# Optimization experiments

Hardware: AMD Instinct MI355X
Metric: run time of the kernel (lower is better)

Reference implementation:

```python
import jax, jax.numpy as jnp
import numpy as np

B, N, ENC = 64, 49, 2048
DEC, ATT, EMB, V, TP1 = 512, 512, 300, 10000, 31


def setup_inputs() -> dict:
    key = jax.random.key(0)
    ks = jax.random.split(key, 20)
    s = 0.02
    inp = {
        "features": jax.random.normal(ks[0], (B, N, ENC), jnp.float32),
        "captions": jax.random.randint(ks[1], (B, TP1), 0, V, jnp.int64),
        "emb": jax.random.normal(ks[2], (V, EMB), jnp.float32) * s,
        "U_w": jax.random.normal(ks[3], (ATT, ENC), jnp.float32) * s,
        "U_b": jnp.zeros((ATT,), jnp.float32),
        "W_w": jax.random.normal(ks[4], (ATT, DEC), jnp.float32) * s,
        "W_b": jnp.zeros((ATT,), jnp.float32),
        "A_w": jax.random.normal(ks[5], (1, ATT), jnp.float32) * s,
        "A_b": jnp.zeros((1,), jnp.float32),
        "initH_w": jax.random.normal(ks[6], (DEC, ENC), jnp.float32) * s,
        "initH_b": jnp.zeros((DEC,), jnp.float32),
        "initC_w": jax.random.normal(ks[7], (DEC, ENC), jnp.float32) * s,
        "initC_b": jnp.zeros((DEC,), jnp.float32),
        "ih_w": jax.random.normal(ks[8], (4 * DEC, EMB + ENC), jnp.float32) * s,
        "ih_b": jnp.zeros((4 * DEC,), jnp.float32),
        "hh_w": jax.random.normal(ks[9], (4 * DEC, DEC), jnp.float32) * s,
        "hh_b": jnp.zeros((4 * DEC,), jnp.float32),
        "fcn_w": jax.random.normal(ks[10], (V, DEC), jnp.float32) * s,
        "fcn_b": jnp.zeros((V,), jnp.float32),
    }
    return inp


def reference(features, captions, emb, U_w, U_b, W_w, W_b, A_w, A_b,
              initH_w, initH_b, initC_w, initC_b,
              ih_w, ih_b, hh_w, hh_b, fcn_w, fcn_b):
    # embeds: [B, T+1, EMB]  (prembed lookup, frozen table)
    embeds = emb[captions]
    T = captions.shape[1] - 1  # static

    # init_hidden_state
    mean_f = features.mean(axis=1)                  # [B, ENC]
    h0 = mean_f @ initH_w.T + initH_b               # [B, DEC]
    c0 = mean_f @ initC_w.T + initC_b

    # U(features) is step-invariant: hoist out of the loop (same math)
    u_hs = jnp.einsum('bne,ae->bna', features, U_w) + U_b  # [B, N, ATT]

    xs = jnp.swapaxes(embeds[:, :T], 0, 1)          # [T, B, EMB]

    def step(carry, x):
        h, c = carry
        # additive attention
        w_ah = h @ W_w.T + W_b                       # [B, ATT]
        comb = jnp.tanh(u_hs + w_ah[:, None, :])     # [B, N, ATT]
        scores = jnp.einsum('bna,a->bn', comb, A_w[0]) + A_b[0]
        alpha = jax.nn.softmax(scores, axis=1)       # [B, N]
        context = jnp.einsum('bn,bne->be', alpha, features)  # [B, ENC]
        # LSTMCell
        lstm_in = jnp.concatenate([x, context], axis=1)
        gates = lstm_in @ ih_w.T + ih_b + h @ hh_w.T + hh_b
        i, f, g, o = jnp.split(gates, 4, axis=1)
        i, f, o = jax.nn.sigmoid(i), jax.nn.sigmoid(f), jax.nn.sigmoid(o)
        g = jnp.tanh(g)
        c = f * c + i * g
        h = o * jnp.tanh(c)
        # dropout in eval mode = identity
        out = h @ fcn_w.T + fcn_b                    # [B, V]
        return (h, c), (out, alpha)

    _, (preds, alphas) = jax.lax.scan(step, (h0, c0), xs)
    preds = jnp.swapaxes(preds, 0, 1)                # [B, T, V]
    alphas = jnp.swapaxes(alphas, 0, 1)              # [B, T, N]
    return preds, alphas
```

## Files before the change

### kernel.cpp

```cpp
#include <hip/hip_runtime.h>
#include <math.h>

#define B 64
#define NN 49
#define ENC 2048
#define DEC 512
#define ATT 512
#define EMB 300
#define VOC 10000
#define TT 30

typedef __attribute__((ext_vector_type(4))) float f32x4;
typedef __attribute__((ext_vector_type(4))) short s16x4;
typedef __attribute__((ext_vector_type(8))) short s16x8;
typedef unsigned short u16;

__device__ __forceinline__ float fast_tanh(float x) {
    float e = __expf(2.f * x);
    return 1.f - 2.f / (e + 1.f);
}
__device__ __forceinline__ float sigmoidf(float x) {
    return 1.f / (1.f + __expf(-x));
}
__device__ __forceinline__ u16 f2bf(float x) {
    unsigned u = __float_as_uint(x);
    unsigned r = u + 0x7FFFu + ((u >> 16) & 1u);
    return (u16)(r >> 16);
}
__device__ __forceinline__ float bf2f(u16 u) {
    return __uint_as_float((unsigned)u << 16);
}
__device__ __forceinline__ void split_bf16(float x, short& hi, short& lo) {
    u16 h = f2bf(x);
    float hf = __uint_as_float((unsigned)h << 16);
    hi = (short)h;
    lo = (short)f2bf(x - hf);
}
__device__ __forceinline__ s16x8 ld8(const short* p) {
    s16x4 a = *(const s16x4*)p;
    s16x4 b = *(const s16x4*)(p + 4);
    return __builtin_shufflevector(a, b, 0, 1, 2, 3, 4, 5, 6, 7);
}
__device__ __forceinline__ int xcd_swz(int bid, int nwg) {
    const int q = nwg >> 3, r = nwg & 7;
    const int xcd = bid & 7, idx = bid >> 3;
    return ((xcd < r) ? xcd * (q + 1) : r * (q + 1) + (xcd - r) * q) + idx;
}

__global__ __launch_bounds__(512) void mfma_cat3(
    const u16* __restrict__ fhi,
    const float* __restrict__ U_w, const float* __restrict__ U_b,
    const u16* __restrict__ ihw_h, const u16* __restrict__ ihw_l,
    u16* __restrict__ uhs16, u16* __restrict__ fW16, int M)
{
    __shared__ short Ah[128][40];
    __shared__ short Bh[128][40];
    __shared__ short Bl[128][40];

    const int tid = threadIdx.x;
    const int nwg = gridDim.x * gridDim.y;
    const int swz = xcd_swz(blockIdx.y * gridDim.x + blockIdx.x, nwg);
    const int m0 = (swz / gridDim.x) * 128;
    const int n0 = (swz % gridDim.x) * 128;
    const int wid = tid >> 6, lane = tid & 63;
    const int wm = wid >> 2, wn = wid & 3;
    const int lrow = lane & 15;
    const int lko = (lane >> 4) * 8;
    const int srow = tid >> 2;
    const int sk = (tid & 3) * 8;

    const int gc = n0 + srow;
    const int gr = m0 + srow;
    const u16* ahp = fhi + (size_t)gr * 2048;

    f32x4 acc[4][2];
    #pragma unroll
    for (int i = 0; i < 4; ++i)
        #pragma unroll
        for (int j = 0; j < 2; ++j)
            acc[i][j] = (f32x4){0.f, 0.f, 0.f, 0.f};

    for (int kt = 0; kt < 64; ++kt) {
        const int kb0 = kt * 32 + sk;
        {
            s16x8 vh = {0,0,0,0,0,0,0,0};
            if (gr < M) vh = *(const s16x8*)(ahp + kb0);
            *(s16x8*)&Ah[srow][sk] = vh;
        }
        if (n0 < 512) {
            const float* bp = U_w + (size_t)gc * 2048;
            float4 x0 = *(const float4*)(bp + kb0);
            float4 x1 = *(const float4*)(bp + kb0 + 4);
            float v[8] = {x0.x, x0.y, x0.z, x0.w, x1.x, x1.y, x1.z, x1.w};
            s16x4 h0, h1, l0, l1;
            #pragma unroll
            for (int j = 0; j < 4; ++j) { short h, l; split_bf16(v[j], h, l); h0[j] = h; l0[j] = l; }
            #pragma unroll
            for (int j = 0; j < 4; ++j) { short h, l; split_bf16(v[4 + j], h, l); h1[j] = h; l1[j] = l; }
            *(s16x4*)&Bh[srow][sk] = h0; *(s16x4*)&Bh[srow][sk + 4] = h1;
            *(s16x4*)&Bl[srow][sk] = l0; *(s16x4*)&Bl[srow][sk + 4] = l1;
        } else {
            *(s16x8*)&Bh[srow][sk] = *(const s16x8*)(ihw_h + (size_t)(gc - 512) * 2048 + kb0);
            *(s16x8*)&Bl[srow][sk] = *(const s16x8*)(ihw_l + (size_t)(gc - 512) * 2048 + kb0);
        }
        __syncthreads();

        s16x8 bh[2], bl[2];
        #pragma unroll
        for (int nr = 0; nr < 2; ++nr) {
            const int col = wn * 32 + nr * 16 + lrow;
            bh[nr] = ld8(&Bh[col][lko]);
            bl[nr] = ld8(&Bl[col][lko]);
        }
        #pragma unroll
        for (int mr = 0; mr < 4; ++mr) {
            const int row = wm * 64 + mr * 16 + lrow;
            s16x8 ah = ld8(&Ah[row][lko]);
            #pragma unroll
            for (int nr = 0; nr < 2; ++nr) {
                acc[mr][nr] = __builtin_amdgcn_mfma_f32_16x16x32_bf16(ah, bh[nr], acc[mr][nr], 0, 0, 0);
                acc[mr][nr] = __builtin_amdgcn_mfma_f32_16x16x32_bf16(ah, bl[nr], acc[mr][nr], 0, 0, 0);
            }
        }
        __syncthreads();
    }

    #pragma unroll
    for (int mr = 0; mr < 4; ++mr) {
        #pragma unroll
        for (int nr = 0; nr < 2; ++nr) {
            #pragma unroll
            for (int r = 0; r < 4; ++r) {
                const int row = m0 + wm * 64 + mr * 16 + (lane >> 4) * 4 + r;
                const int col = n0 + wn * 32 + nr * 16 + (lane & 15);
                if (row < M) {
                    if (col < 512)
                        uhs16[(size_t)row * 512 + col] = f2bf(acc[mr][nr][r] + U_b[col]);
                    else
                        fW16[(size_t)row * 2048 + (col - 512)] = f2bf(acc[mr][nr][r]);
                }
            }
        }
    }
}

__global__ __launch_bounds__(512) void mfma_prex(
    const int* __restrict__ cap,
    const float* __restrict__ emb,
    const float* __restrict__ ih_w,
    const float* __restrict__ bias2,
    float* __restrict__ pre_x)
{
    __shared__ short Ah[128][40];
    __shared__ short Al[128][40];
    __shared__ short Bh[128][40];
    __shared__ short Bl[128][40];

    const int tid = threadIdx.x;
    const int m0 = blockIdx.y * 128, n0 = blockIdx.x * 128;
    const int wid = tid >> 6, lane = tid & 63;
    const int wm = wid >> 2, wn = wid & 3;
    const int lrow = lane & 15;
    const int lko = (lane >> 4) * 8;
    const int srow = tid >> 2;
    const int sk = (tid & 3) * 8;

    const int gr = m0 + srow;
    const int tt = gr >> 6, bbs = gr & 63;
    const float* ap = emb + (size_t)cap[bbs * 31 + tt] * 300;
    const int gc = n0 + srow;
    const float* bp = ih_w + (size_t)gc * 2348;

    f32x4 acc[4][2];
    #pragma unroll
    for (int i = 0; i < 4; ++i)
        #pragma unroll
        for (int j = 0; j < 2; ++j)
            acc[i][j] = (f32x4){0.f, 0.f, 0.f, 0.f};

    for (int kt = 0; kt < 10; ++kt) {
        const int kb0 = kt * 32 + sk;
        {
            float v[8];
            if (kb0 + 7 < 300) {
                float4 x0 = *(const float4*)(ap + kb0);
                float4 x1 = *(const float4*)(ap + kb0 + 4);
                v[0] = x0.x; v[1] = x0.y; v[2] = x0.z; v[3] = x0.w;
                v[4] = x1.x; v[5] = x1.y; v[6] = x1.z; v[7] = x1.w;
            } else {
                #pragma unroll
                for (int j = 0; j < 8; ++j)
                    v[j] = (kb0 + j < 300) ? ap[kb0 + j] : 0.f;
            }
            s16x4 h0, h1, l0, l1;
            #pragma unroll
            for (int j = 0; j < 4; ++j) { short h, l; split_bf16(v[j], h, l); h0[j] = h; l0[j] = l; }
            #pragma unroll
            for (int j = 0; j < 4; ++j) { short h, l; split_bf16(v[4 + j], h, l); h1[j] = h; l1[j] = l; }
            *(s16x4*)&Ah[srow][sk] = h0; *(s16x4*)&Ah[srow][sk + 4] = h1;
            *(s16x4*)&Al[srow][sk] = l0; *(s16x4*)&Al[srow][sk + 4] = l1;
        }
        {
            float v[8];
            if (kb0 + 7 < 300) {
                float4 x0 = *(const float4*)(bp + kb0);
                float4 x1 = *(const float4*)(bp + kb0 + 4);
                v[0] = x0.x; v[1] = x0.y; v[2] = x0.z; v[3] = x0.w;
                v[4] = x1.x; v[5] = x1.y; v[6] = x1.z; v[7] = x1.w;
            } else {
                #pragma unroll
                for (int j = 0; j < 8; ++j)
                    v[j] = (kb0 + j < 300) ? bp[kb0 + j] : 0.f;
            }
            s16x4 h0, h1, l0, l1;
            #pragma unroll
            for (int j = 0; j < 4; ++j) { short h, l; split_bf16(v[j], h, l); h0[j] = h; l0[j] = l; }
            #pragma unroll
            for (int j = 0; j < 4; ++j) { short h, l; split_bf16(v[4 + j], h, l); h1[j] = h; l1[j] = l; }
            *(s16x4*)&Bh[srow][sk] = h0; *(s16x4*)&Bh[srow][sk + 4] = h1;
            *(s16x4*)&Bl[srow][sk] = l0; *(s16x4*)&Bl[srow][sk + 4] = l1;
        }
        __syncthreads();

        s16x8 bh[2], bl[2];
        #pragma unroll
        for (int nr = 0; nr < 2; ++nr) {
            const int col = wn * 32 + nr * 16 + lrow;
            bh[nr] = ld8(&Bh[col][lko]);
            bl[nr] = ld8(&Bl[col][lko]);
        }
        #pragma unroll
        for (int mr = 0; mr < 4; ++mr) {
            const int row = wm * 64 + mr * 16 + lrow;
            s16x8 ah = ld8(&Ah[row][lko]);
            s16x8 al = ld8(&Al[row][lko]);
            #pragma unroll
            for (int nr = 0; nr < 2; ++nr) {
                acc[mr][nr] = __builtin_amdgcn_mfma_f32_16x16x32_bf16(ah, bh[nr], acc[mr][nr], 0, 0, 0);
                acc[mr][nr] = __builtin_amdgcn_mfma_f32_16x16x32_bf16(ah, bl[nr], acc[mr][nr], 0, 0, 0);
                acc[mr][nr] = __builtin_amdgcn_mfma_f32_16x16x32_bf16(al, bh[nr], acc[mr][nr], 0, 0, 0);
            }
        }
        __syncthreads();
    }

    #pragma unroll
    for (int mr = 0; mr < 4; ++mr) {
        #pragma unroll
        for (int nr = 0; nr < 2; ++nr) {
            #pragma unroll
            for (int r = 0; r < 4; ++r) {
                const int row = m0 + wm * 64 + mr * 16 + (lane >> 4) * 4 + r;
                const int col = n0 + wn * 32 + nr * 16 + (lane & 15);
                pre_x[(size_t)row * 2048 + col] = acc[mr][nr][r] + bias2[col];
            }
        }
    }
}

__global__ __launch_bounds__(512) void mfma_pre3(
    const u16* __restrict__ Ahg,
    const u16* __restrict__ Bhg,
    const float* __restrict__ bias,
    float* __restrict__ C, int M, int N)
{
    __shared__ short Ah[128][40];
    __shared__ short Bh[128][40];

    const int tid = threadIdx.x;
    const int nwg = gridDim.x * gridDim.y;
    const int swz = xcd_swz(blockIdx.y * gridDim.x + blockIdx.x, nwg);
    const int m0 = (swz / gridDim.x) * 128;
    const int n0 = (swz % gridDim.x) * 128;
    const int wid = tid >> 6, lane = tid & 63;
    const int wm = wid >> 2, wn = wid & 3;
    const int lrow = lane & 15;
    const int lko = (lane >> 4) * 8;
    const int srow = tid >> 2;
    const int sk = (tid & 3) * 8;

    f32x4 acc[4][2];
    #pragma unroll
    for (int i = 0; i < 4; ++i)
        #pragma unroll
        for (int j = 0; j < 2; ++j)
            acc[i][j] = (f32x4){0.f, 0.f, 0.f, 0.f};

    for (int kt = 0; kt < 16; ++kt) {
        const int kb0 = kt * 32 + sk;
        {
            const int gr = m0 + srow;
            s16x8 vh = {0,0,0,0,0,0,0,0};
            if (gr < M) vh = *(const s16x8*)(Ahg + (size_t)gr * 512 + kb0);
            *(s16x8*)&Ah[srow][sk] = vh;
        }
        {
            const int gc = n0 + srow;
            s16x8 vh = {0,0,0,0,0,0,0,0};
            if (gc < N) vh = *(const s16x8*)(Bhg + (size_t)gc * 512 + kb0);
            *(s16x8*)&Bh[srow][sk] = vh;
        }
        __syncthreads();

        s16x8 bh[2];
        #pragma unroll
        for (int nr = 0; nr < 2; ++nr) {
            const int col = wn * 32 + nr * 16 + lrow;
            bh[nr] = ld8(&Bh[col][lko]);
        }
        #pragma unroll
        for (int mr = 0; mr < 4; ++mr) {
            const int row = wm * 64 + mr * 16 + lrow;
            s16x8 ah = ld8(&Ah[row][lko]);
            #pragma unroll
            for (int nr = 0; nr < 2; ++nr)
                acc[mr][nr] = __builtin_amdgcn_mfma_f32_16x16x32_bf16(ah, bh[nr], acc[mr][nr], 0, 0, 0);
        }
        __syncthreads();
    }

    #pragma unroll
    for (int mr = 0; mr < 4; ++mr) {
        #pragma unroll
        for (int nr = 0; nr < 2; ++nr) {
            #pragma unroll
            for (int r = 0; r < 4; ++r) {
                const int row = m0 + wm * 64 + mr * 16 + (lane >> 4) * 4 + r;
                const int col = n0 + wn * 32 + nr * 16 + (lane & 15);
                if (row < M && col < N) {
                    const float val = acc[mr][nr][r] + bias[col];
                    const int t = row >> 6, bb = row & 63;
                    C[(size_t)bb * (TT * VOC) + (size_t)t * VOC + col] = val;
                }
            }
        }
    }
}

__global__ __launch_bounds__(256) void k_mean(const float* __restrict__ f,
                                              float* __restrict__ mean_f)
{
    const int b = blockIdx.x;
    for (int e = threadIdx.x; e < ENC; e += 256) {
        float s = 0.f;
        for (int n = 0; n < NN; ++n) s += f[(size_t)(b * NN + n) * ENC + e];
        mean_f[(size_t)b * ENC + e] = s * (1.f / 49.f);
    }
}

__global__ __launch_bounds__(256) void k_init_partial(
    const float* __restrict__ mean_f,
    const float* __restrict__ iH_w, const float* __restrict__ iC_w,
    float* __restrict__ pbuf)
{
    const int tid = threadIdx.x;
    const int tx = tid & 15, ty = tid >> 4;
    const int n0 = blockIdx.x * 64;
    const int ks = blockIdx.y;
    __shared__ float As[16][64];
    __shared__ float Bs[16][64];
    float acc[4][4] = {};
    const int lrow = tid >> 2;
    const int lk = (tid & 3) * 4;
    for (int c = 0; c < 8; ++c) {
        const int kk = ks * 128 + c * 16 + lk;
        float4 av = *(const float4*)(mean_f + (size_t)lrow * 2048 + kk);
        const int col = n0 + lrow;
        const float* wp = (col < 512) ? (iH_w + (size_t)col * 2048)
                                      : (iC_w + (size_t)(col - 512) * 2048);
        float4 bv = *(const float4*)(wp + kk);
        As[lk + 0][lrow] = av.x; As[lk + 1][lrow] = av.y;
        As[lk + 2][lrow] = av.z; As[lk + 3][lrow] = av.w;
        Bs[lk + 0][lrow] = bv.x; Bs[lk + 1][lrow] = bv.y;
        Bs[lk + 2][lrow] = bv.z; Bs[lk + 3][lrow] = bv.w;
        __syncthreads();
        #pragma unroll
        for (int k = 0; k < 16; ++k) {
            float4 a = *(const float4*)&As[k][ty * 4];
            float4 b = *(const float4*)&Bs[k][tx * 4];
            acc[0][0] += a.x * b.x; acc[0][1] += a.x * b.y; acc[0][2] += a.x * b.z; acc[0][3] += a.x * b.w;
            acc[1][0] += a.y * b.x; acc[1][1] += a.y * b.y; acc[1][2] += a.y * b.z; acc[1][3] += a.y * b.w;
            acc[2][0] += a.z * b.x; acc[2][1] += a.z * b.y; acc[2][2] += a.z * b.z; acc[2][3] += a.z * b.w;
            acc[3][0] += a.w * b.x; acc[3][1] += a.w * b.y; acc[3][2] += a.w * b.z; acc[3][3] += a.w * b.w;
        }
        __syncthreads();
    }
    #pragma unroll
    for (int i = 0; i < 4; ++i) {
        const int r = ty * 4 + i;
        #pragma unroll
        for (int j = 0; j < 4; ++j)
            pbuf[(size_t)(ks * 64 + r) * 1024 + n0 + tx * 4 + j] = acc[i][j];
    }
}

__global__ __launch_bounds__(256) void k_init_reduce(
    const float* __restrict__ pbuf,
    const float* __restrict__ iH_b, const float* __restrict__ iC_b,
    float* __restrict__ h_cur, float* __restrict__ c_cur)
{
    const int idx = blockIdx.x * 256 + threadIdx.x;
    const int r = idx >> 10, c = idx & 1023;
    float s = 0.f;
    #pragma unroll
    for (int ks = 0; ks < 16; ++ks) s += pbuf[(size_t)(ks * 64 + r) * 1024 + c];
    if (c < 512) h_cur[r * 512 + c] = s + iH_b[c];
    else         c_cur[r * 512 + (c - 512)] = s + iC_b[c - 512];
}

__global__ __launch_bounds__(256) void k_prep(
    const float* __restrict__ ih_w, const float* __restrict__ fcn_w,
    const float* __restrict__ features,
    const float* __restrict__ ih_b, const float* __restrict__ hh_b,
    u16* __restrict__ ihw_h, u16* __restrict__ ihw_l,
    u16* __restrict__ fcnw_h, u16* __restrict__ fhi,
    float* __restrict__ bias2)
{
    const int bid = blockIdx.x;
    const int tid = threadIdx.x;
    if (bid < 2048) {
        const float* src = ih_w + (size_t)bid * 2348 + 300;
        u16* hp = ihw_h + (size_t)bid * 2048;
        u16* lp = ihw_l + (size_t)bid * 2048;
        const int c = tid * 8;
        #pragma unroll
        for (int g = 0; g < 2; ++g) {
            f32x4 v = *(const f32x4*)(src + c + g * 4);
            s16x4 h4, l4;
            #pragma unroll
            for (int j = 0; j < 4; ++j) { short h, l; split_bf16(v[j], h, l); h4[j] = h; l4[j] = l; }
            *(s16x4*)(hp + c + g * 4) = h4;
            *(s16x4*)(lp + c + g * 4) = l4;
        }
    } else if (bid < 4548) {
        const int i = (bid - 2048) * 2048 + tid * 8;
        #pragma unroll
        for (int g = 0; g < 2; ++g) {
            f32x4 v = *(const f32x4*)(fcn_w + i + g * 4);
            s16x4 h4;
            #pragma unroll
            for (int j = 0; j < 4; ++j) h4[j] = (short)f2bf(v[j]);
            *(s16x4*)(fcnw_h + i + g * 4) = h4;
        }
    } else if (bid < 6116) {
        const int i = (bid - 4548) * 4096 + tid * 16;
        #pragma unroll
        for (int g = 0; g < 4; ++g) {
            f32x4 v = *(const f32x4*)(features + i + g * 4);
            s16x4 h4;
            #pragma unroll
            for (int j = 0; j < 4; ++j) h4[j] = (short)f2bf(v[j]);
            *(s16x4*)(fhi + i + g * 4) = h4;
        }
    } else {
        const int j = tid * 8;
        #pragma unroll
        for (int k = 0; k < 8; ++k) bias2[j + k] = ih_b[j + k] + hh_b[j + k];
    }
}

__global__ __launch_bounds__(256) void k_hw8(
    const float* __restrict__ h,
    const float* __restrict__ W_w, const float* __restrict__ W_b,
    const float* __restrict__ hh_w,
    float* __restrict__ wahp, float* __restrict__ ghhp)
{
    const int tid = threadIdx.x;
    const int tx = tid & 15, ty = tid >> 4;
    const int n0 = blockIdx.x * 64;
    const int ks = blockIdx.y;
    const float* Bp; const float* biasp; float* Cp; int c0, ldc;
    if (n0 < 512) { Bp = W_w + (size_t)n0 * 512; biasp = (ks == 0) ? W_b : nullptr; Cp = wahp + (size_t)ks * 32768; c0 = n0; ldc = 512; }
    else { Bp = hh_w + (size_t)(n0 - 512) * 512; biasp = nullptr; Cp = ghhp + (size_t)ks * 131072; c0 = n0 - 512; ldc = 2048; }

    __shared__ float As[64][68];
    __shared__ float Bs[64][68];
    float acc[4][4] = {};
    const int rt = tid >> 2;
    const int cs = (tid & 3) * 16;
    const int kbase = ks * 64;

    #pragma unroll
    for (int i = 0; i < 4; ++i) {
        const int c = cs + i * 4;
        *(f32x4*)&As[rt][c] = *(const f32x4*)(h + (size_t)rt * 512 + kbase + c);
        *(f32x4*)&Bs[rt][c] = *(const f32x4*)(Bp + (size_t)rt * 512 + kbase + c);
    }
    __syncthreads();
    #pragma unroll 4
    for (int k4 = 0; k4 < 16; ++k4) {
        f32x4 a0 = *(const f32x4*)&As[ty + 0][k4 * 4];
        f32x4 a1 = *(const f32x4*)&As[ty + 16][k4 * 4];
        f32x4 a2 = *(const f32x4*)&As[ty + 32][k4 * 4];
        f32x4 a3 = *(const f32x4*)&As[ty + 48][k4 * 4];
        f32x4 b0 = *(const f32x4*)&Bs[tx + 0][k4 * 4];
        f32x4 b1 = *(const f32x4*)&Bs[tx + 16][k4 * 4];
        f32x4 b2 = *(const f32x4*)&Bs[tx + 32][k4 * 4];
        f32x4 b3 = *(const f32x4*)&Bs[tx + 48][k4 * 4];
        #pragma unroll
        for (int e = 0; e < 4; ++e) {
            acc[0][0] += a0[e] * b0[e]; acc[0][1] += a0[e] * b1[e];
            acc[0][2] += a0[e] * b2[e]; acc[0][3] += a0[e] * b3[e];
            acc[1][0] += a1[e] * b0[e]; acc[1][1] += a1[e] * b1[e];
            acc[1][2] += a1[e] * b2[e]; acc[1][3] += a1[e] * b3[e];
            acc[2][0] += a2[e] * b0[e]; acc[2][1] += a2[e] * b1[e];
            acc[2][2] += a2[e] * b2[e]; acc[2][3] += a2[e] * b3[e];
            acc[3][0] += a3[e] * b0[e]; acc[3][1] += a3[e] * b1[e];
            acc[3][2] += a3[e] * b2[e]; acc[3][3] += a3[e] * b3[e];
        }
    }
    #pragma unroll
    for (int i = 0; i < 4; ++i) {
        const int r = ty + i * 16;
        #pragma unroll
        for (int j = 0; j < 4; ++j) {
            const int cc = c0 + tx + j * 16;
            Cp[(size_t)r * ldc + cc] = acc[i][j] + (biasp ? biasp[cc] : 0.f);
        }
    }
}

__global__ __launch_bounds__(512) void k_fused6(
    const u16* __restrict__ uhs16,
    const float* __restrict__ A_w, const float* __restrict__ A_b,
    const float* __restrict__ wahp,
    const float* __restrict__ ghhp,
    const float* __restrict__ pre_x,
    const u16* __restrict__ fW16,
    float* __restrict__ h_cur, float* __restrict__ c_cur,
    u16* __restrict__ Hall_h,
    float* __restrict__ alphas, int s)
{
    const int bb = blockIdx.x;
    const int qq = blockIdx.y;
    const int tid = threadIdx.x;
    const int lane = tid & 63, w = tid >> 6;
    __shared__ float wah_l[512];
    __shared__ float red[64];
    __shared__ float al[64];
    __shared__ float ghl[512];
    __shared__ float gl[512];

    const int gate = tid >> 7, dloc = tid & 127;
    const int jcol = gate * 512 + qq * 128 + dloc;
    float ghv = pre_x[(size_t)(s * 64 + bb) * 2048 + jcol];
    #pragma unroll
    for (int i = 0; i < 8; ++i)
        ghv += ghhp[(size_t)i * 131072 + (size_t)bb * 2048 + jcol];
    float wv = 0.f;
    #pragma unroll
    for (int i = 0; i < 8; ++i)
        wv += wahp[(size_t)i * 32768 + bb * 512 + tid];
    const float cload = c_cur[bb * 512 + qq * 128 + (tid & 127)];

    const int a0 = lane * 8;
    float aw8[8];
    #pragma unroll
    for (int k = 0; k < 8; ++k) aw8[k] = A_w[a0 + k];

    const int ngf = tid & 7, r = tid >> 3;
    const int gf = r >> 4, oc = r & 15;
    const int jb = gf * 512 + qq * 128 + oc * 8;
    const u16* fb = fW16 + (size_t)bb * NN * 2048 + jb;
    s16x8 pf[7];
    #pragma unroll
    for (int i = 0; i < 7; ++i) {
        const int n = ngf + 8 * i;
        if (n < NN) pf[i] = *(const s16x8*)(fb + (size_t)n * 2048);
        else        pf[i] = (s16x8){0, 0, 0, 0, 0, 0, 0, 0};
    }

    ghl[tid] = ghv;
    wah_l[tid] = wv;
    __syncthreads();

    float wh8[8];
    #pragma unroll
    for (int k = 0; k < 8; ++k) wh8[k] = wah_l[a0 + k];

    const u16* ub = uhs16 + (size_t)(bb * NN) * 512 + a0;
    #pragma unroll
    for (int i = 0; i < 7; ++i) {
        const int n = w + 8 * i;
        const int nc = (n < NN) ? n : 0;
        const s16x8 uv = *(const s16x8*)(ub + (size_t)nc * 512);
        float acc = 0.f;
        #pragma unroll
        for (int k = 0; k < 8; ++k)
            acc += aw8[k] * fast_tanh(bf2f((u16)uv[k]) + wh8[k]);
        #pragma unroll
        for (int m = 32; m; m >>= 1) acc += __shfl_xor(acc, m, 64);
        if (lane == 0 && n < NN) red[n] = acc + A_b[0];
    }
    __syncthreads();

    if (tid < 64) {
        const float sc = (tid < NN) ? red[tid] : -1e30f;
        float mx = sc;
        #pragma unroll
        for (int m = 32; m; m >>= 1) mx = fmaxf(mx, __shfl_xor(mx, m, 64));
        float e = (tid < NN) ? __expf(sc - mx) : 0.f;
        float sum = e;
        #pragma unroll
        for (int m = 32; m; m >>= 1) sum += __shfl_xor(sum, m, 64);
        const float av = e / sum;
        al[tid] = av;
        if (qq == 0 && tid < NN)
            alphas[(size_t)bb * (TT * NN) + (size_t)s * NN + tid] = av;
    }
    __syncthreads();

    float a8[8] = {0.f, 0.f, 0.f, 0.f, 0.f, 0.f, 0.f, 0.f};
    #pragma unroll
    for (int i = 0; i < 7; ++i) {
        const int n = ngf + 8 * i;
        const float av = al[n];
        #pragma unroll
        for (int k = 0; k < 8; ++k)
            a8[k] += av * bf2f((u16)pf[i][k]);
    }
    #pragma unroll
    for (int m = 1; m < 8; m <<= 1)
        #pragma unroll
        for (int k = 0; k < 8; ++k)
            a8[k] += __shfl_xor(a8[k], m, 64);
    if (ngf == 0) {
        const int base = gf * 128 + oc * 8;
        #pragma unroll
        for (int k = 0; k < 8; ++k)
            gl[base + k] = a8[k] + ghl[base + k];
    }
    __syncthreads();

    if (tid < 128) {
        const int dd = qq * 128 + tid;
        const float ig = sigmoidf(gl[tid]);
        const float fg = sigmoidf(gl[128 + tid]);
        const float gg = fast_tanh(gl[256 + tid]);
        const float og = sigmoidf(gl[384 + tid]);
        const float cv = fg * cload + ig * gg;
        const float hv = og * fast_tanh(cv);
        c_cur[bb * 512 + dd] = cv;
        h_cur[bb * 512 + dd] = hv;
        Hall_h[(size_t)(s * 64 + bb) * 512 + dd] = f2bf(hv);
    }
}

extern "C" void kernel_launch(void* const* d_in, const int* in_sizes, int n_in,
                              void* d_out, int out_size, void* d_ws, size_t ws_size,
                              hipStream_t stream)
{
    const float* features = (const float*)d_in[0];
    const int*   captions = (const int*)d_in[1];
    const float* emb      = (const float*)d_in[2];
    const float* U_w      = (const float*)d_in[3];
    const float* U_b      = (const float*)d_in[4];
    const float* W_w      = (const float*)d_in[5];
    const float* W_b      = (const float*)d_in[6];
    const float* A_w      = (const float*)d_in[7];
    const float* A_b      = (const float*)d_in[8];
    const float* iH_w     = (const float*)d_in[9];
    const float* iH_b     = (const float*)d_in[10];
    const float* iC_w     = (const float*)d_in[11];
    const float* iC_b     = (const float*)d_in[12];
    const float* ih_w     = (const float*)d_in[13];
    const float* ih_b     = (const float*)d_in[14];
    const float* hh_w     = (const float*)d_in[15];
    const float* hh_b     = (const float*)d_in[16];
    const float* fcn_w    = (const float*)d_in[17];
    const float* fcn_b    = (const float*)d_in[18];

    float* out    = (float*)d_out;
    float* alphas = out + (size_t)B * TT * VOC;

    float* ws     = (float*)d_ws;
    u16*  fW16    = (u16*)ws;
    u16*  uhs16   = (u16*)(ws + 3211264);
    float* pre_x  = ws + 4014080;
    u16*  Hall_h  = (u16*)(ws + 7946240);
    float* h_cur  = ws + 8437760;
    float* c_cur  = ws + 8470528;
    float* wahp   = ws + 8503296;
    float* ghhp   = ws + 8765440;
    float* bias2  = ws + 9814016;
    u16*  fhi     = (u16*)(ws + 9816064);
    u16*  fcnw_h  = (u16*)(ws + 13027328);
    float* pbuf   = ws;
    float* mean_f = ws + 1048576;
    u16*  ihw_h   = (u16*)pre_x;
    u16*  ihw_l   = (u16*)(ws + 6111232);

    k_mean<<<64, 256, 0, stream>>>(features, mean_f);
    k_init_partial<<<dim3(16, 16), 256, 0, stream>>>(mean_f, iH_w, iC_w, pbuf);
    k_init_reduce<<<256, 256, 0, stream>>>(pbuf, iH_b, iC_b, h_cur, c_cur);

    k_prep<<<6117, 256, 0, stream>>>(ih_w, fcn_w, features, ih_b, hh_b,
                                     ihw_h, ihw_l, fcnw_h, fhi, bias2);

    mfma_cat3<<<dim3(20, 25), 512, 0, stream>>>(fhi, U_w, U_b, ihw_h, ihw_l,
                                                uhs16, fW16, B * NN);
    mfma_prex<<<dim3(16, 15), 512, 0, stream>>>(captions, emb, ih_w, bias2, pre_x);

    k_hw8<<<dim3(40, 8), 256, 0, stream>>>(h_cur, W_w, W_b, hh_w, wahp, ghhp);
    for (int s = 0; s < TT; ++s) {
        k_fused6<<<dim3(64, 4), 512, 0, stream>>>(uhs16, A_w, A_b, wahp, ghhp, pre_x, fW16,
                                                  h_cur, c_cur, Hall_h, alphas, s);
        if (s < TT - 1)
            k_hw8<<<dim3(40, 8), 256, 0, stream>>>(h_cur, W_w, W_b, hh_w, wahp, ghhp);
    }

    mfma_pre3<<<dim3(79, 15), 512, 0, stream>>>(Hall_h, fcnw_h, fcn_b,
                                                out, TT * B, VOC);
}
```

Measured before the change: 846.5 us.

## Replace per-step recurrent launches with persistent kernel using global barriers

The 59 per-timestep launches (k_hw8 plus k_fused6) are replaced by one persistent 256-block kernel that runs all 30 steps, syncing through an atomic-counter grid barrier. Each block computes its slice of the h·W and h·hh products in fp32 with h staged in swizzled LDS, then does the attention, context and LSTM update as before. The c state stays in registers and h goes to per-step buffers. Separately, the fcn_w bf16 conversion moves from the prep pass into the final vocab GEMM's tile load. This removes launch overhead and partial-sum buffers, but relies on all 256 blocks being co-resident and adds per-element conversion work to the output GEMM.

```diff
diff --git a/kernel.cpp b/kernel.cpp
--- a/kernel.cpp
+++ b/kernel.cpp
@@ -9,6 +9,7 @@
 #define EMB 300
 #define VOC 10000
 #define TT 30
+#define NBLK 256
 
 typedef __attribute__((ext_vector_type(4))) float f32x4;
 typedef __attribute__((ext_vector_type(4))) short s16x4;
@@ -258,9 +259,9 @@
     }
 }
 
-__global__ __launch_bounds__(512) void mfma_pre3(
+__global__ __launch_bounds__(512) void mfma_pre4(
     const u16* __restrict__ Ahg,
-    const u16* __restrict__ Bhg,
+    const float* __restrict__ Bf,
     const float* __restrict__ bias,
     float* __restrict__ C, int M, int N)
 {
@@ -296,9 +297,18 @@
         }
         {
             const int gc = n0 + srow;
-            s16x8 vh = {0,0,0,0,0,0,0,0};
-            if (gc < N) vh = *(const s16x8*)(Bhg + (size_t)gc * 512 + kb0);
-            *(s16x8*)&Bh[srow][sk] = vh;
+            s16x4 h0 = {0,0,0,0}, h1 = {0,0,0,0};
+            if (gc < N) {
+                const float* bp = Bf + (size_t)gc * 512 + kb0;
+                float4 x0 = *(const float4*)bp;
+                float4 x1 = *(const float4*)(bp + 4);
+                h0[0] = (short)f2bf(x0.x); h0[1] = (short)f2bf(x0.y);
+                h0[2] = (short)f2bf(x0.z); h0[3] = (short)f2bf(x0.w);
+                h1[0] = (short)f2bf(x1.x); h1[1] = (short)f2bf(x1.y);
+                h1[2] = (short)f2bf(x1.z); h1[3] = (short)f2bf(x1.w);
+            }
+            *(s16x4*)&Bh[srow][sk] = h0;
+            *(s16x4*)&Bh[srow][sk + 4] = h1;
         }
         __syncthreads();
 
@@ -409,11 +419,11 @@
 }
 
 __global__ __launch_bounds__(256) void k_prep(
-    const float* __restrict__ ih_w, const float* __restrict__ fcn_w,
+    const float* __restrict__ ih_w,
     const float* __restrict__ features,
     const float* __restrict__ ih_b, const float* __restrict__ hh_b,
     u16* __restrict__ ihw_h, u16* __restrict__ ihw_l,
-    u16* __restrict__ fcnw_h, u16* __restrict__ fhi,
+    u16* __restrict__ fhi,
     float* __restrict__ bias2)
 {
     const int bid = blockIdx.x;
@@ -432,18 +442,8 @@
             *(s16x4*)(hp + c + g * 4) = h4;
             *(s16x4*)(lp + c + g * 4) = l4;
         }
-    } else if (bid < 4548) {
-        const int i = (bid - 2048) * 2048 + tid * 8;
-        #pragma unroll
-        for (int g = 0; g < 2; ++g) {
-            f32x4 v = *(const f32x4*)(fcn_w + i + g * 4);
-            s16x4 h4;
-            #pragma unroll
-            for (int j = 0; j < 4; ++j) h4[j] = (short)f2bf(v[j]);
-            *(s16x4*)(fcnw_h + i + g * 4) = h4;
-        }
-    } else if (bid < 6116) {
-        const int i = (bid - 4548) * 4096 + tid * 16;
+    } else if (bid < 3616) {
+        const int i = (bid - 2048) * 4096 + tid * 16;
         #pragma unroll
         for (int g = 0; g < 4; ++g) {
             f32x4 v = *(const f32x4*)(features + i + g * 4);
@@ -459,190 +459,200 @@
     }
 }
 
-__global__ __launch_bounds__(256) void k_hw8(
-    const float* __restrict__ h,
+__global__ void k_zero(unsigned* __restrict__ p) { p[0] = 0u; }
+
+struct SBC {
+    float wah[512];
+    float red[64];
+    float al[64];
+    float ghl[512];
+    float gl[512];
+};
+union SU {
+    float h[64][256];
+    SBC bc;
+};
+
+__device__ __forceinline__ void gbar(unsigned* cnt, unsigned target) {
+    __syncthreads();
+    if (threadIdx.x == 0) {
+        __hip_atomic_fetch_add(cnt, 1u, __ATOMIC_RELEASE, __HIP_MEMORY_SCOPE_AGENT);
+        while (__hip_atomic_load(cnt, __ATOMIC_RELAXED, __HIP_MEMORY_SCOPE_AGENT) < target)
+            __builtin_amdgcn_s_sleep(1);
+    }
+    __syncthreads();
+}
+
+__global__ __launch_bounds__(512) void k_recur2(
     const float* __restrict__ W_w, const float* __restrict__ W_b,
     const float* __restrict__ hh_w,
-    float* __restrict__ wahp, float* __restrict__ ghhp)
-{
-    const int tid = threadIdx.x;
-    const int tx = tid & 15, ty = tid >> 4;
-    const int n0 = blockIdx.x * 64;
-    const int ks = blockIdx.y;
-    const float* Bp; const float* biasp; float* Cp; int c0, ldc;
-    if (n0 < 512) { Bp = W_w + (size_t)n0 * 512; biasp = (ks == 0) ? W_b : nullptr; Cp = wahp + (size_t)ks * 32768; c0 = n0; ldc = 512; }
-    else { Bp = hh_w + (size_t)(n0 - 512) * 512; biasp = nullptr; Cp = ghhp + (size_t)ks * 131072; c0 = n0 - 512; ldc = 2048; }
-
-    __shared__ float As[64][68];
-    __shared__ float Bs[64][68];
-    float acc[4][4] = {};
-    const int rt = tid >> 2;
-    const int cs = (tid & 3) * 16;
-    const int kbase = ks * 64;
-
-    #pragma unroll
-    for (int i = 0; i < 4; ++i) {
-        const int c = cs + i * 4;
-        *(f32x4*)&As[rt][c] = *(const f32x4*)(h + (size_t)rt * 512 + kbase + c);
-        *(f32x4*)&Bs[rt][c] = *(const f32x4*)(Bp + (size_t)rt * 512 + kbase + c);
-    }
-    __syncthreads();
-    #pragma unroll 4
-    for (int k4 = 0; k4 < 16; ++k4) {
-        f32x4 a0 = *(const f32x4*)&As[ty + 0][k4 * 4];
-        f32x4 a1 = *(const f32x4*)&As[ty + 16][k4 * 4];
-        f32x4 a2 = *(const f32x4*)&As[ty + 32][k4 * 4];
-        f32x4 a3 = *(const f32x4*)&As[ty + 48][k4 * 4];
-        f32x4 b0 = *(const f32x4*)&Bs[tx + 0][k4 * 4];
-        f32x4 b1 = *(const f32x4*)&Bs[tx + 16][k4 * 4];
-        f32x4 b2 = *(const f32x4*)&Bs[tx + 32][k4 * 4];
-        f32x4 b3 = *(const f32x4*)&Bs[tx + 48][k4 * 4];
-        #pragma unroll
-        for (int e = 0; e < 4; ++e) {
-            acc[0][0] += a0[e] * b0[e]; acc[0][1] += a0[e] * b1[e];
-            acc[0][2] += a0[e] * b2[e]; acc[0][3] += a0[e] * b3[e];
-            acc[1][0] += a1[e] * b0[e]; acc[1][1] += a1[e] * b1[e];
-            acc[1][2] += a1[e] * b2[e]; acc[1][3] += a1[e] * b3[e];
-            acc[2][0] += a2[e] * b0[e]; acc[2][1] += a2[e] * b1[e];
-            acc[2][2] += a2[e] * b2[e]; acc[2][3] += a2[e] * b3[e];
-            acc[3][0] += a3[e] * b0[e]; acc[3][1] += a3[e] * b1[e];
-            acc[3][2] += a3[e] * b2[e]; acc[3][3] += a3[e] * b3[e];
-        }
-    }
-    #pragma unroll
-    for (int i = 0; i < 4; ++i) {
-        const int r = ty + i * 16;
-        #pragma unroll
-        for (int j = 0; j < 4; ++j) {
-            const int cc = c0 + tx + j * 16;
-            Cp[(size_t)r * ldc + cc] = acc[i][j] + (biasp ? biasp[cc] : 0.f);
-        }
-    }
-}
-
-__global__ __launch_bounds__(512) void k_fused6(
-    const u16* __restrict__ uhs16,
     const float* __restrict__ A_w, const float* __restrict__ A_b,
-    const float* __restrict__ wahp,
-    const float* __restrict__ ghhp,
-    const float* __restrict__ pre_x,
+    const u16* __restrict__ uhs16, const float* __restrict__ pre_x,
     const u16* __restrict__ fW16,
-    float* __restrict__ h_cur, float* __restrict__ c_cur,
-    u16* __restrict__ Hall_h,
-    float* __restrict__ alphas, int s)
-{
-    const int bb = blockIdx.x;
-    const int qq = blockIdx.y;
+    const float* __restrict__ h0, const float* __restrict__ c0,
+    float* __restrict__ wahghs,
+    float* __restrict__ hbufs,
+    u16* __restrict__ Hall_h, float* __restrict__ alphas,
+    unsigned* __restrict__ cnt)
+{
+    __shared__ SU sm;
+    const int g = blockIdx.x;
     const int tid = threadIdx.x;
     const int lane = tid & 63, w = tid >> 6;
-    __shared__ float wah_l[512];
-    __shared__ float red[64];
-    __shared__ float al[64];
-    __shared__ float ghl[512];
-    __shared__ float gl[512];
+    const int bb = g & 63, qq = g >> 6;
+    unsigned tgt = 0;
 
     const int gate = tid >> 7, dloc = tid & 127;
     const int jcol = gate * 512 + qq * 128 + dloc;
-    float ghv = pre_x[(size_t)(s * 64 + bb) * 2048 + jcol];
-    #pragma unroll
-    for (int i = 0; i < 8; ++i)
-        ghv += ghhp[(size_t)i * 131072 + (size_t)bb * 2048 + jcol];
-    float wv = 0.f;
-    #pragma unroll
-    for (int i = 0; i < 8; ++i)
-        wv += wahp[(size_t)i * 32768 + bb * 512 + tid];
-    const float cload = c_cur[bb * 512 + qq * 128 + (tid & 127)];
-
     const int a0 = lane * 8;
-    float aw8[8];
-    #pragma unroll
-    for (int k = 0; k < 8; ++k) aw8[k] = A_w[a0 + k];
-
-    const int ngf = tid & 7, r = tid >> 3;
-    const int gf = r >> 4, oc = r & 15;
+    const int ngf = tid & 7, rr = tid >> 3;
+    const int gf = rr >> 4, oc = rr & 15;
     const int jb = gf * 512 + qq * 128 + oc * 8;
     const u16* fb = fW16 + (size_t)bb * NN * 2048 + jb;
-    s16x8 pf[7];
-    #pragma unroll
-    for (int i = 0; i < 7; ++i) {
-        const int n = ngf + 8 * i;
-        if (n < NN) pf[i] = *(const s16x8*)(fb + (size_t)n * 2048);
-        else        pf[i] = (s16x8){0, 0, 0, 0, 0, 0, 0, 0};
-    }
-
-    ghl[tid] = ghv;
-    wah_l[tid] = wv;
-    __syncthreads();
-
-    float wh8[8];
-    #pragma unroll
-    for (int k = 0; k < 8; ++k) wh8[k] = wah_l[a0 + k];
-
-    const u16* ub = uhs16 + (size_t)(bb * NN) * 512 + a0;
-    #pragma unroll
-    for (int i = 0; i < 7; ++i) {
-        const int n = w + 8 * i;
-        const int nc = (n < NN) ? n : 0;
-        const s16x8 uv = *(const s16x8*)(ub + (size_t)nc * 512);
-        float acc = 0.f;
-        #pragma unroll
-        for (int k = 0; k < 8; ++k)
-            acc += aw8[k] * fast_tanh(bf2f((u16)uv[k]) + wh8[k]);
-        #pragma unroll
-        for (int m = 32; m; m >>= 1) acc += __shfl_xor(acc, m, 64);
-        if (lane == 0 && n < NN) red[n] = acc + A_b[0];
-    }
-    __syncthreads();
-
-    if (tid < 64) {
-        const float sc = (tid < NN) ? red[tid] : -1e30f;
-        float mx = sc;
-        #pragma unroll
-        for (int m = 32; m; m >>= 1) mx = fmaxf(mx, __shfl_xor(mx, m, 64));
-        float e = (tid < NN) ? __expf(sc - mx) : 0.f;
-        float sum = e;
-        #pragma unroll
-        for (int m = 32; m; m >>= 1) sum += __shfl_xor(sum, m, 64);
-        const float av = e / sum;
-        al[tid] = av;
-        if (qq == 0 && tid < NN)
-            alphas[(size_t)bb * (TT * NN) + (size_t)s * NN + tid] = av;
-    }
-    __syncthreads();
-
-    float a8[8] = {0.f, 0.f, 0.f, 0.f, 0.f, 0.f, 0.f, 0.f};
-    #pragma unroll
-    for (int i = 0; i < 7; ++i) {
-        const int n = ngf + 8 * i;
-        const float av = al[n];
-        #pragma unroll
-        for (int k = 0; k < 8; ++k)
-            a8[k] += av * bf2f((u16)pf[i][k]);
-    }
-    #pragma unroll
-    for (int m = 1; m < 8; m <<= 1)
-        #pragma unroll
-        for (int k = 0; k < 8; ++k)
-            a8[k] += __shfl_xor(a8[k], m, 64);
-    if (ngf == 0) {
-        const int base = gf * 128 + oc * 8;
-        #pragma unroll
-        for (int k = 0; k < 8; ++k)
-            gl[base + k] = a8[k] + ghl[base + k];
-    }
-    __syncthreads();
-
-    if (tid < 128) {
-        const int dd = qq * 128 + tid;
-        const float ig = sigmoidf(gl[tid]);
-        const float fg = sigmoidf(gl[128 + tid]);
-        const float gg = fast_tanh(gl[256 + tid]);
-        const float og = sigmoidf(gl[384 + tid]);
-        const float cv = fg * cload + ig * gg;
-        const float hv = og * fast_tanh(cv);
-        c_cur[bb * 512 + dd] = cv;
-        h_cur[bb * 512 + dd] = hv;
-        Hall_h[(size_t)(s * 64 + bb) * 512 + dd] = f2bf(hv);
+    float aw8[8];
+    #pragma unroll
+    for (int k = 0; k < 8; ++k) aw8[k] = A_w[a0 + k];
+    float cv = (tid < 128) ? c0[bb * 512 + qq * 128 + tid] : 0.f;
+
+    const int base = g * 10;
+    const int C0 = base + w;
+    const int C1 = (w < 2) ? (base + 8 + w) : -1;
+    const int swl = (lane & 7) << 2;
+
+    for (int s = 0; s < TT; ++s) {
+        const float* hsrc = (s == 0) ? h0 : (hbufs + (size_t)(s - 1) * 32768);
+        float* wg = wahghs + (size_t)s * 163840;
+
+        {
+            float acc0 = 0.f, acc1 = 0.f;
+            for (int kh = 0; kh < 2; ++kh) {
+                __syncthreads();
+                {
+                    const int b = tid >> 3;
+                    const int k0 = (tid & 7) * 32;
+                    const float* src = hsrc + b * 512 + kh * 256 + k0;
+                    const int sw = (b & 7) << 2;
+                    #pragma unroll
+                    for (int i = 0; i < 8; ++i)
+                        *(f32x4*)&sm.h[b][(k0 + i * 4) ^ sw] = *(const f32x4*)(src + i * 4);
+                }
+                __syncthreads();
+                {
+                    const int C0u = __builtin_amdgcn_readfirstlane(C0);
+                    const float* wr0 = ((C0u < 512) ? (W_w + (size_t)C0u * 512)
+                                                    : (hh_w + (size_t)(C0u - 512) * 512)) + kh * 256;
+                    const float* wr1 = nullptr;
+                    if (C1 >= 0) {
+                        const int C1u = __builtin_amdgcn_readfirstlane(C1);
+                        wr1 = ((C1u < 512) ? (W_w + (size_t)C1u * 512)
+                                           : (hh_w + (size_t)(C1u - 512) * 512)) + kh * 256;
+                    }
+                    #pragma unroll 4
+                    for (int k = 0; k < 256; k += 4) {
+                        f32x4 hv = *(const f32x4*)&sm.h[lane][k ^ swl];
+                        f32x4 wv0 = *(const f32x4*)(wr0 + k);
+                        acc0 += wv0[0] * hv[0] + wv0[1] * hv[1] + wv0[2] * hv[2] + wv0[3] * hv[3];
+                        if (wr1) {
+                            f32x4 wv1 = *(const f32x4*)(wr1 + k);
+                            acc1 += wv1[0] * hv[0] + wv1[1] * hv[1] + wv1[2] * hv[2] + wv1[3] * hv[3];
+                        }
+                    }
+                }
+            }
+            wg[lane * 2560 + C0] = acc0 + ((C0 < 512) ? W_b[C0] : 0.f);
+            if (C1 >= 0)
+                wg[lane * 2560 + C1] = acc1 + ((C1 < 512) ? W_b[C1] : 0.f);
+        }
+        tgt += NBLK; gbar(cnt, tgt);
+
+        {
+            float ghv = pre_x[(size_t)(s * 64 + bb) * 2048 + jcol]
+                      + wg[bb * 2560 + 512 + jcol];
+            float wv = wg[bb * 2560 + tid];
+
+            s16x8 pf[7];
+            #pragma unroll
+            for (int i = 0; i < 7; ++i) {
+                const int n = ngf + 8 * i;
+                if (n < NN) pf[i] = *(const s16x8*)(fb + (size_t)n * 2048);
+                else        pf[i] = (s16x8){0, 0, 0, 0, 0, 0, 0, 0};
+            }
+
+            sm.bc.ghl[tid] = ghv;
+            sm.bc.wah[tid] = wv;
+            __syncthreads();
+
+            float wh8[8];
+            #pragma unroll
+            for (int k = 0; k < 8; ++k) wh8[k] = sm.bc.wah[a0 + k];
+
+            const u16* ub = uhs16 + (size_t)(bb * NN) * 512 + a0;
+            #pragma unroll
+            for (int i = 0; i < 7; ++i) {
+                const int n = w + 8 * i;
+                const int nc = (n < NN) ? n : 0;
+                const s16x8 uv = *(const s16x8*)(ub + (size_t)nc * 512);
+                float acc = 0.f;
+                #pragma unroll
+                for (int k = 0; k < 8; ++k)
+                    acc += aw8[k] * fast_tanh(bf2f((u16)uv[k]) + wh8[k]);
+                #pragma unroll
+                for (int m = 32; m; m >>= 1) acc += __shfl_xor(acc, m, 64);
+                if (lane == 0 && n < NN) sm.bc.red[n] = acc + A_b[0];
+            }
+            __syncthreads();
+
+            if (tid < 64) {
+                const float sc = (tid < NN) ? sm.bc.red[tid] : -1e30f;
+                float mx = sc;
+                #pragma unroll
+                for (int m = 32; m; m >>= 1) mx = fmaxf(mx, __shfl_xor(mx, m, 64));
+                float e = (tid < NN) ? __expf(sc - mx) : 0.f;
+                float sum = e;
+                #pragma unroll
+                for (int m = 32; m; m >>= 1) sum += __shfl_xor(sum, m, 64);
+                const float av = e / sum;
+                sm.bc.al[tid] = av;
+                if (qq == 0 && tid < NN)
+                    alphas[(size_t)bb * (TT * NN) + (size_t)s * NN + tid] = av;
+            }
+            __syncthreads();
+
+            float a8[8] = {0.f, 0.f, 0.f, 0.f, 0.f, 0.f, 0.f, 0.f};
+            #pragma unroll
+            for (int i = 0; i < 7; ++i) {
+                const int n = ngf + 8 * i;
+                const float av = sm.bc.al[n];
+                #pragma unroll
+                for (int k = 0; k < 8; ++k)
+                    a8[k] += av * bf2f((u16)pf[i][k]);
+            }
+            #pragma unroll
+            for (int m = 1; m < 8; m <<= 1)
+                #pragma unroll
+                for (int k = 0; k < 8; ++k)
+                    a8[k] += __shfl_xor(a8[k], m, 64);
+            if (ngf == 0) {
+                const int bidx = gf * 128 + oc * 8;
+                #pragma unroll
+                for (int k = 0; k < 8; ++k)
+                    sm.bc.gl[bidx + k] = a8[k] + sm.bc.ghl[bidx + k];
+            }
+            __syncthreads();
+
+            if (tid < 128) {
+                const int dd = qq * 128 + tid;
+                const float ig = sigmoidf(sm.bc.gl[tid]);
+                const float fg = sigmoidf(sm.bc.gl[128 + tid]);
+                const float gg = fast_tanh(sm.bc.gl[256 + tid]);
+                const float og = sigmoidf(sm.bc.gl[384 + tid]);
+                cv = fg * cv + ig * gg;
+                const float hv = og * fast_tanh(cv);
+                hbufs[(size_t)s * 32768 + bb * 512 + dd] = hv;
+                Hall_h[(size_t)(s * 64 + bb) * 512 + dd] = f2bf(hv);
+            }
+        }
+        tgt += NBLK; gbar(cnt, tgt);
     }
 }
 
@@ -678,37 +688,34 @@
     u16*  uhs16   = (u16*)(ws + 3211264);
     float* pre_x  = ws + 4014080;
     u16*  Hall_h  = (u16*)(ws + 7946240);
-    float* h_cur  = ws + 8437760;
-    float* c_cur  = ws + 8470528;
-    float* wahp   = ws + 8503296;
-    float* ghhp   = ws + 8765440;
-    float* bias2  = ws + 9814016;
-    u16*  fhi     = (u16*)(ws + 9816064);
-    u16*  fcnw_h  = (u16*)(ws + 13027328);
+    float* h0     = ws + 8437760;
+    float* c0     = ws + 8470528;
+    float* bias2  = ws + 8503296;
+    unsigned* cnt = (unsigned*)(ws + 8505344);
+    float* wahghs = ws + 8505408;
+    float* hbufs  = ws + 13420608;
     float* pbuf   = ws;
     float* mean_f = ws + 1048576;
     u16*  ihw_h   = (u16*)pre_x;
     u16*  ihw_l   = (u16*)(ws + 6111232);
+    u16*  fhi     = (u16*)(ws + 8505408);
 
     k_mean<<<64, 256, 0, stream>>>(features, mean_f);
     k_init_partial<<<dim3(16, 16), 256, 0, stream>>>(mean_f, iH_w, iC_w, pbuf);
-    k_init_reduce<<<256, 256, 0, stream>>>(pbuf, iH_b, iC_b, h_cur, c_cur);
-
-    k_prep<<<6117, 256, 0, stream>>>(ih_w, fcn_w, features, ih_b, hh_b,
-                                     ihw_h, ihw_l, fcnw_h, fhi, bias2);
+    k_init_reduce<<<256, 256, 0, stream>>>(pbuf, iH_b, iC_b, h0, c0);
+
+    k_prep<<<3617, 256, 0, stream>>>(ih_w, features, ih_b, hh_b,
+                                     ihw_h, ihw_l, fhi, bias2);
+    k_zero<<<1, 1, 0, stream>>>(cnt);
 
     mfma_cat3<<<dim3(20, 25), 512, 0, stream>>>(fhi, U_w, U_b, ihw_h, ihw_l,
                                                 uhs16, fW16, B * NN);
     mfma_prex<<<dim3(16, 15), 512, 0, stream>>>(captions, emb, ih_w, bias2, pre_x);
 
-    k_hw8<<<dim3(40, 8), 256, 0, stream>>>(h_cur, W_w, W_b, hh_w, wahp, ghhp);
-    for (int s = 0; s < TT; ++s) {
-        k_fused6<<<dim3(64, 4), 512, 0, stream>>>(uhs16, A_w, A_b, wahp, ghhp, pre_x, fW16,
-                                                  h_cur, c_cur, Hall_h, alphas, s);
-        if (s < TT - 1)
-            k_hw8<<<dim3(40, 8), 256, 0, stream>>>(h_cur, W_w, W_b, hh_w, wahp, ghhp);
-    }
-
-    mfma_pre3<<<dim3(79, 15), 512, 0, stream>>>(Hall_h, fcnw_h, fcn_b,
+    k_recur2<<<NBLK, 512, 0, stream>>>(W_w, W_b, hh_w, A_w, A_b,
+                                       uhs16, pre_x, fW16, h0, c0,
+                                       wahghs, hbufs, Hall_h, alphas, cnt);
+
+    mfma_pre4<<<dim3(79, 15), 512, 0, stream>>>(Hall_h, fcn_w, fcn_b,
                                                 out, TT * B, VOC);
 }
```

After: 1.991 ms. 2.35x slower.
